# Kernel optimization log

Hardware: AMD Instinct MI355X
Metric: run time of the kernel (lower is better)

Reference implementation:

```python
import jax, jax.numpy as jnp
import numpy as np

N_NODES = 100000
IN_CH = 128
HID = 16
N_EDGES = 3200000


def setup_inputs() -> dict:
    key = jax.random.key(0)
    k1, k2, k3, k4 = jax.random.split(key, 4)
    x = jax.random.normal(k1, (N_NODES, IN_CH), dtype=jnp.float32)
    edge_index = jax.random.randint(k2, (2, N_EDGES), 0, N_NODES, dtype=jnp.int64)
    s1 = 1.0 / np.sqrt(IN_CH)
    s2 = 1.0 / np.sqrt(HID)
    W1 = jax.random.uniform(k3, (IN_CH, HID), dtype=jnp.float32, minval=-s1, maxval=s1)
    b1 = jnp.zeros((HID,), dtype=jnp.float32)
    W2 = jax.random.uniform(k4, (HID, HID), dtype=jnp.float32, minval=-s2, maxval=s2)
    b2 = jnp.zeros((HID,), dtype=jnp.float32)
    return {"x": x, "edge_index": edge_index, "W1": W1, "b1": b1, "W2": W2, "b2": b2}


def _gcn_layer(h, W, b, row, col, norm, n_nodes):
    # GCNConv: transform first (small hidden dim), then normalized sum aggregation
    h = h @ W  # [N, out]
    msg = h[row] * norm[:, None]  # gather over edges incl. self-loops
    out = jax.ops.segment_sum(msg, col, num_segments=n_nodes)
    return out + b


def reference(x, edge_index, W1, b1, W2, b2):
    n = x.shape[0]
    row, col = edge_index[0], edge_index[1]
    # add self-loops (PyG GCNConv default)
    loop = jnp.arange(n, dtype=edge_index.dtype)
    row_l = jnp.concatenate([row, loop])
    col_l = jnp.concatenate([col, loop])
    # symmetric normalization D^-1/2 (A+I) D^-1/2 (degree from target index)
    deg = jax.ops.segment_sum(jnp.ones_like(col_l, dtype=x.dtype), col_l, num_segments=n)
    dinv = jnp.where(deg > 0, jax.lax.rsqrt(deg), 0.0)
    norm = dinv[row_l] * dinv[col_l]

    h = _gcn_layer(x, W1, b1, row_l, col_l, norm, n)
    h = jax.nn.relu(h)  # dropout is identity at eval
    h = _gcn_layer(h, W2, b2, row_l, col_l, norm, n)

    # fused per-edge dot-product link score + sigmoid (original edges only)
    scores = jnp.sum(h[row] * h[col], axis=-1)
    return jax.nn.sigmoid(scores)
```

## Files before the change

kernel.cpp:

```cpp
#include <hip/hip_runtime.h>
#include <hip/hip_bf16.h>
#include <hip/hip_fp16.h>
#include <math.h>


#define BSH 9
#define BSZ 512
#define MAXCH 3200
#define MAXCHUNKS 1024

__global__ __launch_bounds__(512) void pA(const int* __restrict__ col,
                                          int* __restrict__ M, int E, int CH, int NBUK) {
    __shared__ int hist[256];
    const int t = threadIdx.x, b = blockIdx.x;
    if (t < 256) hist[t] = 0;
    __syncthreads();
    const int s = b * CH, e = min(E, s + CH);
    const int n4 = (e - s) >> 2;
    const int4* c4 = (const int4*)(col + s);
    for (int i = t; i < n4; i += 512) {
        int4 c = c4[i];
        atomicAdd(&hist[c.x >> BSH], 1);
        atomicAdd(&hist[c.y >> BSH], 1);
        atomicAdd(&hist[c.z >> BSH], 1);
        atomicAdd(&hist[c.w >> BSH], 1);
    }
    for (int i = s + (n4 << 2) + t; i < e; i += 512) atomicAdd(&hist[col[i] >> BSH], 1);
    __syncthreads();
    for (int i = t; i < NBUK; i += 512) M[b * NBUK + i] = hist[i];
}

__global__ __launch_bounds__(1024) void pB1(int* __restrict__ M, int* __restrict__ T,
                                            int NBUK, int CN) {
    __shared__ int s[1024];
    const int t = threadIdx.x, k = blockIdx.x;
    int own = (t < CN) ? M[t * NBUK + k] : 0;
    s[t] = own;
    __syncthreads();
    for (int d = 1; d < 1024; d <<= 1) {
        int add = (t >= d) ? s[t - d] : 0;
        __syncthreads();
        s[t] += add;
        __syncthreads();
    }
    if (t < CN) M[t * NBUK + k] = s[t] - own;
    if (t == 1023) T[k] = s[1023];
}

__global__ __launch_bounds__(512) void pB2(const int* __restrict__ T, int* __restrict__ S,
                                           int* __restrict__ start, int NBUK, int N, int E) {
    __shared__ int s[512];
    const int t = threadIdx.x;
    int own = (t < NBUK) ? T[t] : 0;
    s[t] = own;
    __syncthreads();
    for (int d = 1; d < 512; d <<= 1) {
        int add = (t >= d) ? s[t - d] : 0;
        __syncthreads();
        s[t] += add;
        __syncthreads();
    }
    if (t < NBUK) S[t] = s[t] - own;
    if (t == 511) S[NBUK] = s[511];
    if (t == 0) start[N] = E;
}

__global__ __launch_bounds__(512) void pC(const int* __restrict__ row, const int* __restrict__ col,
                                          const int* __restrict__ M, const int* __restrict__ S,
                                          unsigned int* __restrict__ ebuf, int E, int CH, int NBUK) {
    __shared__ unsigned int se[MAXCH];
    __shared__ unsigned short pk[MAXCH];
    __shared__ int lhist[256], lbase[256], lcur[256], gbase[256];
    const int t = threadIdx.x, b = blockIdx.x;
    if (t < 256) lhist[t] = 0;
    __syncthreads();
    const int s = b * CH, e = min(E, s + CH);
    const int cnt = e - s;
    const int n4 = cnt >> 2;
    const int4* c4 = (const int4*)(col + s);
    const int4* r4 = (const int4*)(row + s);
    for (int i = t; i < n4; i += 512) {
        int4 c = c4[i];
        atomicAdd(&lhist[c.x >> BSH], 1);
        atomicAdd(&lhist[c.y >> BSH], 1);
        atomicAdd(&lhist[c.z >> BSH], 1);
        atomicAdd(&lhist[c.w >> BSH], 1);
    }
    for (int i = (n4 << 2) + t; i < cnt; i += 512) atomicAdd(&lhist[col[s + i] >> BSH], 1);
    __syncthreads();
    {
        int own = (t < 256) ? lhist[t] : 0;
        if (t < 256) lcur[t] = own;
        __syncthreads();
        for (int d = 1; d < 256; d <<= 1) {
            int add = (t < 256 && t >= d) ? lcur[t - d] : 0;
            __syncthreads();
            if (t < 256) lcur[t] += add;
            __syncthreads();
        }
        if (t < 256) {
            lbase[t] = lcur[t] - own;
            lcur[t] = lcur[t] - own;
        }
        __syncthreads();
        if (t < NBUK) gbase[t] = S[t] + M[b * NBUK + t] - lbase[t];
    }
    __syncthreads();
    for (int i = t; i < n4; i += 512) {
        int4 c = c4[i];
        int4 r = r4[i];
        int k0 = c.x >> BSH, p0 = atomicAdd(&lcur[k0], 1);
        se[p0] = ((unsigned int)(c.x & (BSZ - 1)) << 17) | (unsigned int)r.x; pk[p0] = (unsigned short)k0;
        int k1 = c.y >> BSH, p1 = atomicAdd(&lcur[k1], 1);
        se[p1] = ((unsigned int)(c.y & (BSZ - 1)) << 17) | (unsigned int)r.y; pk[p1] = (unsigned short)k1;
        int k2 = c.z >> BSH, p2 = atomicAdd(&lcur[k2], 1);
        se[p2] = ((unsigned int)(c.z & (BSZ - 1)) << 17) | (unsigned int)r.z; pk[p2] = (unsigned short)k2;
        int k3 = c.w >> BSH, p3 = atomicAdd(&lcur[k3], 1);
        se[p3] = ((unsigned int)(c.w & (BSZ - 1)) << 17) | (unsigned int)r.w; pk[p3] = (unsigned short)k3;
    }
    for (int i = (n4 << 2) + t; i < cnt; i += 512) {
        int c = col[s + i], r = row[s + i];
        int k = c >> BSH, p = atomicAdd(&lcur[k], 1);
        se[p] = ((unsigned int)(c & (BSZ - 1)) << 17) | (unsigned int)r; pk[p] = (unsigned short)k;
    }
    __syncthreads();
    for (int i = t; i < cnt; i += 512) {
        int k = pk[i];
        ebuf[gbase[k] + i] = se[i];
    }
}

__global__ __launch_bounds__(1024) void pC2(const unsigned int* __restrict__ ebuf,
                                            const int* __restrict__ S,
                                            unsigned int* __restrict__ ebuf2,
                                            float* __restrict__ dinv,
                                            int* __restrict__ start, int N) {
    __shared__ int h[BSZ], sc[BSZ], cur[BSZ];
    const int t = threadIdx.x, k = blockIdx.x;
    if (t < BSZ) h[t] = 0;
    __syncthreads();
    const int s = S[k], e = S[k + 1];
    for (int i = s + t; i < e; i += 1024) atomicAdd(&h[ebuf[i] >> 17], 1);
    __syncthreads();
    if (t < BSZ) sc[t] = h[t];
    __syncthreads();
    for (int d = 1; d < BSZ; d <<= 1) {
        int add = (t < BSZ && t >= d) ? sc[t - d] : 0;
        __syncthreads();
        if (t < BSZ) sc[t] += add;
        __syncthreads();
    }
    if (t < BSZ) {
        cur[t] = sc[t] - h[t];
        const int v = (k << BSH) + t;
        if (v < N) {
            dinv[v] = rsqrtf((float)h[t] + 1.0f);
            start[v] = s + cur[t];
        }
    }
    __syncthreads();
    for (int i = s + t; i < e; i += 1024) {
        unsigned int w = ebuf[i];
        int p = atomicAdd(&cur[w >> 17], 1);
        ebuf2[s + p] = w;
    }
}

__global__ __launch_bounds__(256) void k_gemm1(
    const float* __restrict__ x, const float* __restrict__ W1,
    const float* __restrict__ dinv, __half* __restrict__ ts, int N) {
    __shared__ float wsT[16 * 132];
    const int tid = threadIdx.x;
    for (int idx = tid; idx < 2048; idx += 256) {
        int k = idx >> 4, c = idx & 15;
        wsT[c * 132 + k] = W1[idx];
    }
    __syncthreads();
    const int n = blockIdx.x * 256 + tid;
    if (n >= N) return;
    const float4* xr = (const float4*)(x + (size_t)n * 128);
    float acc[16];
    #pragma unroll
    for (int c = 0; c < 16; ++c) acc[c] = 0.f;
    #pragma unroll 4
    for (int k4 = 0; k4 < 32; ++k4) {
        float4 a = xr[k4];
        #pragma unroll
        for (int c = 0; c < 16; ++c) {
            const float4 w = *(const float4*)&wsT[c * 132 + k4 * 4];
            acc[c] = fmaf(a.x, w.x, fmaf(a.y, w.y, fmaf(a.z, w.z, fmaf(a.w, w.w, acc[c]))));
        }
    }
    float dv = dinv[n];
    union { __half h[16]; uint4 u[2]; } o;
    #pragma unroll
    for (int c = 0; c < 16; ++c) o.h[c] = __float2half(acc[c] * dv);
    uint4* dst = (uint4*)(ts + (size_t)n * 16);
    dst[0] = o.u[0]; dst[1] = o.u[1];
}

#define ACC8(q) do {                                         \
    float2 f_;                                               \
    f_ = __half22float2(*(const __half2*)&(q).x); a0 += f_.x; a1 += f_.y; \
    f_ = __half22float2(*(const __half2*)&(q).y); a2 += f_.x; a3 += f_.y; \
    f_ = __half22float2(*(const __half2*)&(q).z); a4 += f_.x; a5 += f_.y; \
    f_ = __half22float2(*(const __half2*)&(q).w); a6 += f_.x; a7 += f_.y; \
} while (0)

__global__ __launch_bounds__(256) void pGat1(
    const unsigned int* __restrict__ ebuf2, const int* __restrict__ start,
    const uint4* __restrict__ tsq, const float* __restrict__ dinv,
    const float* __restrict__ b1, const float* __restrict__ W2,
    uint4* __restrict__ ts2q, int N) {
    __shared__ float w2s[256];
    const int tid = threadIdx.x;
    w2s[tid] = W2[tid];
    __syncthreads();
    const int p = tid & 1;
    const int v = blockIdx.x * 128 + (tid >> 1);
    if (v >= N) return;
    const int s = start[v], e = start[v + 1];
    float a0 = 0.f, a1 = 0.f, a2 = 0.f, a3 = 0.f, a4 = 0.f, a5 = 0.f, a6 = 0.f, a7 = 0.f;
    int i = s;
    for (; i + 8 <= e; i += 8) {
        uint4 q0 = tsq[((size_t)(ebuf2[i    ] & 0x1FFFF) << 1) + p];
        uint4 q1 = tsq[((size_t)(ebuf2[i + 1] & 0x1FFFF) << 1) + p];
        uint4 q2 = tsq[((size_t)(ebuf2[i + 2] & 0x1FFFF) << 1) + p];
        uint4 q3 = tsq[((size_t)(ebuf2[i + 3] & 0x1FFFF) << 1) + p];
        uint4 q4 = tsq[((size_t)(ebuf2[i + 4] & 0x1FFFF) << 1) + p];
        uint4 q5 = tsq[((size_t)(ebuf2[i + 5] & 0x1FFFF) << 1) + p];
        uint4 q6 = tsq[((size_t)(ebuf2[i + 6] & 0x1FFFF) << 1) + p];
        uint4 q7 = tsq[((size_t)(ebuf2[i + 7] & 0x1FFFF) << 1) + p];
        ACC8(q0); ACC8(q1); ACC8(q2); ACC8(q3);
        ACC8(q4); ACC8(q5); ACC8(q6); ACC8(q7);
    }
    for (; i + 4 <= e; i += 4) {
        uint4 q0 = tsq[((size_t)(ebuf2[i    ] & 0x1FFFF) << 1) + p];
        uint4 q1 = tsq[((size_t)(ebuf2[i + 1] & 0x1FFFF) << 1) + p];
        uint4 q2 = tsq[((size_t)(ebuf2[i + 2] & 0x1FFFF) << 1) + p];
        uint4 q3 = tsq[((size_t)(ebuf2[i + 3] & 0x1FFFF) << 1) + p];
        ACC8(q0); ACC8(q1); ACC8(q2); ACC8(q3);
    }
    for (; i < e; ++i) {
        uint4 q0 = tsq[((size_t)(ebuf2[i] & 0x1FFFF) << 1) + p];
        ACC8(q0);
    }
    {
        uint4 sq = tsq[((size_t)v << 1) + p];
        ACC8(sq);
    }
    const float dv = dinv[v];
    const float4 bA = ((const float4*)b1)[2 * p];
    const float4 bB = ((const float4*)b1)[2 * p + 1];
    float h[8];
    h[0] = fmaxf(fmaf(dv, a0, bA.x), 0.f);
    h[1] = fmaxf(fmaf(dv, a1, bA.y), 0.f);
    h[2] = fmaxf(fmaf(dv, a2, bA.z), 0.f);
    h[3] = fmaxf(fmaf(dv, a3, bA.w), 0.f);
    h[4] = fmaxf(fmaf(dv, a4, bB.x), 0.f);
    h[5] = fmaxf(fmaf(dv, a5, bB.y), 0.f);
    h[6] = fmaxf(fmaf(dv, a6, bB.z), 0.f);
    h[7] = fmaxf(fmaf(dv, a7, bB.w), 0.f);
    const int my = p * 8, ot = (1 - p) * 8;
    float o[8];
    #pragma unroll
    for (int c = 0; c < 8; ++c) o[c] = 0.f;
    #pragma unroll
    for (int j = 0; j < 8; ++j) {
        float hm = h[j];
        float ho = __shfl_xor(h[j], 1);
        #pragma unroll
        for (int c = 0; c < 8; ++c) {
            o[c] = fmaf(hm, w2s[(my + j) * 16 + my + c],
                   fmaf(ho, w2s[(ot + j) * 16 + my + c], o[c]));
        }
    }
    union { __half hh[8]; uint4 u; } ov;
    #pragma unroll
    for (int c = 0; c < 8; ++c) ov.hh[c] = __float2half(dv * o[c]);
    ts2q[((size_t)v << 1) + p] = ov.u;
}

__global__ __launch_bounds__(256) void pGat2(
    const unsigned int* __restrict__ ebuf2, const int* __restrict__ start,
    const uint4* __restrict__ tsq, const float* __restrict__ dinv,
    const float* __restrict__ b2, uint4* __restrict__ h2q, int N) {
    const int tid = threadIdx.x;
    const int p = tid & 1;
    const int v = blockIdx.x * 128 + (tid >> 1);
    if (v >= N) return;
    const int s = start[v], e = start[v + 1];
    float a0 = 0.f, a1 = 0.f, a2 = 0.f, a3 = 0.f, a4 = 0.f, a5 = 0.f, a6 = 0.f, a7 = 0.f;
    int i = s;
    for (; i + 8 <= e; i += 8) {
        uint4 q0 = tsq[((size_t)(ebuf2[i    ] & 0x1FFFF) << 1) + p];
        uint4 q1 = tsq[((size_t)(ebuf2[i + 1] & 0x1FFFF) << 1) + p];
        uint4 q2 = tsq[((size_t)(ebuf2[i + 2] & 0x1FFFF) << 1) + p];
        uint4 q3 = tsq[((size_t)(ebuf2[i + 3] & 0x1FFFF) << 1) + p];
        uint4 q4 = tsq[((size_t)(ebuf2[i + 4] & 0x1FFFF) << 1) + p];
        uint4 q5 = tsq[((size_t)(ebuf2[i + 5] & 0x1FFFF) << 1) + p];
        uint4 q6 = tsq[((size_t)(ebuf2[i + 6] & 0x1FFFF) << 1) + p];
        uint4 q7 = tsq[((size_t)(ebuf2[i + 7] & 0x1FFFF) << 1) + p];
        ACC8(q0); ACC8(q1); ACC8(q2); ACC8(q3);
        ACC8(q4); ACC8(q5); ACC8(q6); ACC8(q7);
    }
    for (; i + 4 <= e; i += 4) {
        uint4 q0 = tsq[((size_t)(ebuf2[i    ] & 0x1FFFF) << 1) + p];
        uint4 q1 = tsq[((size_t)(ebuf2[i + 1] & 0x1FFFF) << 1) + p];
        uint4 q2 = tsq[((size_t)(ebuf2[i + 2] & 0x1FFFF) << 1) + p];
        uint4 q3 = tsq[((size_t)(ebuf2[i + 3] & 0x1FFFF) << 1) + p];
        ACC8(q0); ACC8(q1); ACC8(q2); ACC8(q3);
    }
    for (; i < e; ++i) {
        uint4 q0 = tsq[((size_t)(ebuf2[i] & 0x1FFFF) << 1) + p];
        ACC8(q0);
    }
    {
        uint4 sq = tsq[((size_t)v << 1) + p];
        ACC8(sq);
    }
    const float dv = dinv[v];
    const float4 bA = ((const float4*)b2)[2 * p];
    const float4 bB = ((const float4*)b2)[2 * p + 1];
    union { __half hh[8]; uint4 u; } ov;
    ov.hh[0] = __float2half(fmaf(dv, a0, bA.x));
    ov.hh[1] = __float2half(fmaf(dv, a1, bA.y));
    ov.hh[2] = __float2half(fmaf(dv, a2, bA.z));
    ov.hh[3] = __float2half(fmaf(dv, a3, bA.w));
    ov.hh[4] = __float2half(fmaf(dv, a4, bB.x));
    ov.hh[5] = __float2half(fmaf(dv, a5, bB.y));
    ov.hh[6] = __float2half(fmaf(dv, a6, bB.z));
    ov.hh[7] = __float2half(fmaf(dv, a7, bB.w));
    h2q[((size_t)v << 1) + p] = ov.u;
}

__global__ void k_score(const int* __restrict__ row, const int* __restrict__ col,
                        const __half* __restrict__ h2h, float* __restrict__ out, int E) {
    int e = blockIdx.x * 256 + threadIdx.x;
    if (e < E) {
        union { uint4 u[2]; __half2 h[8]; } a, b;
        const uint4* pa = (const uint4*)(h2h + (size_t)row[e] * 16);
        const uint4* pb = (const uint4*)(h2h + (size_t)col[e] * 16);
        a.u[0] = pa[0]; a.u[1] = pa[1];
        b.u[0] = pb[0]; b.u[1] = pb[1];
        float d = 0.f;
        #pragma unroll
        for (int i = 0; i < 8; ++i) {
            float2 fa = __half22float2(a.h[i]);
            float2 fb = __half22float2(b.h[i]);
            d = fmaf(fa.x, fb.x, fmaf(fa.y, fb.y, d));
        }
        out[e] = 1.0f / (1.0f + __expf(-d));
    }
}

__global__ void k_countf(const int* __restrict__ col, float* __restrict__ deg, int E) {
    int e = blockIdx.x * 256 + threadIdx.x;
    if (e < E) atomicAdd(&deg[col[e]], 1.0f);
}
__global__ void k_dinvf(float* __restrict__ dinv, int N) {
    int v = blockIdx.x * 256 + threadIdx.x;
    if (v < N) dinv[v] = rsqrtf(dinv[v] + 1.0f);
}
__global__ __launch_bounds__(256) void k_gemm1f(
    const float* __restrict__ x, const float* __restrict__ W1,
    const float* __restrict__ dinv, float* __restrict__ ts, int N) {
    __shared__ float wsT[16 * 132];
    const int tid = threadIdx.x;
    for (int idx = tid; idx < 2048; idx += 256) {
        int k = idx >> 4, c = idx & 15;
        wsT[c * 132 + k] = W1[idx];
    }
    __syncthreads();
    const int n = blockIdx.x * 256 + tid;
    if (n >= N) return;
    const float4* xr = (const float4*)(x + (size_t)n * 128);
    float acc[16];
    #pragma unroll
    for (int c = 0; c < 16; ++c) acc[c] = 0.f;
    for (int k4 = 0; k4 < 32; ++k4) {
        float4 a = xr[k4];
        #pragma unroll
        for (int c = 0; c < 16; ++c) {
            const float4 w = *(const float4*)&wsT[c * 132 + k4 * 4];
            acc[c] = fmaf(a.x, w.x, fmaf(a.y, w.y, fmaf(a.z, w.z, fmaf(a.w, w.w, acc[c]))));
        }
    }
    float dv = dinv[n];
    float4* o = (float4*)(ts + (size_t)n * 16);
    #pragma unroll
    for (int q = 0; q < 4; ++q)
        o[q] = make_float4(acc[4*q] * dv, acc[4*q+1] * dv, acc[4*q+2] * dv, acc[4*q+3] * dv);
}
__global__ void k_scatter(const int* __restrict__ row, const int* __restrict__ col,
                          const float* __restrict__ ts, float* __restrict__ acc, int E) {
    int g = blockIdx.x * 256 + threadIdx.x;
    int e = g >> 4, c = g & 15;
    if (e < E) atomicAdd(&acc[(size_t)col[e] * 16 + c], ts[(size_t)row[e] * 16 + c]);
}
__global__ void k_finalize(float* __restrict__ acc, const float* __restrict__ ts,
                           const float* __restrict__ dinv, const float* __restrict__ b,
                           int N, int relu) {
    int g = blockIdx.x * 256 + threadIdx.x;
    int v = g >> 4, c = g & 15;
    if (v < N) {
        float h = dinv[v] * (acc[g] + ts[g]) + b[c];
        if (relu) h = fmaxf(h, 0.f);
        acc[g] = h;
    }
}
__global__ __launch_bounds__(256) void k_gemm2f(
    const float* __restrict__ h1, const float* __restrict__ W2,
    const float* __restrict__ dinv, float* __restrict__ ts2, int N) {
    __shared__ float hs[16 * 17];
    __shared__ float ws2[256];
    const int tid = threadIdx.x;
    const int base = blockIdx.x * 16;
    if (tid < 64) ((float4*)ws2)[tid] = ((const float4*)W2)[tid];
    if (tid >= 64 && tid < 128) {
        int t2 = tid - 64;
        float4 v4 = ((const float4*)(h1 + (size_t)base * 16))[t2];
        float* d = &hs[(t2 >> 2) * 17 + (t2 & 3) * 4];
        d[0] = v4.x; d[1] = v4.y; d[2] = v4.z; d[3] = v4.w;
    }
    __syncthreads();
    const int r = tid >> 4, c = tid & 15;
    float a = 0.f;
    #pragma unroll
    for (int kk = 0; kk < 16; ++kk) a = fmaf(hs[r * 17 + kk], ws2[kk * 16 + c], a);
    ts2[(size_t)(base + r) * 16 + c] = a * dinv[base + r];
}
__global__ void k_scoref(const int* __restrict__ row, const int* __restrict__ col,
                         const float* __restrict__ h2, float* __restrict__ out, int E) {
    int e = blockIdx.x * 256 + threadIdx.x;
    if (e < E) {
        const float4* a = (const float4*)(h2 + (size_t)row[e] * 16);
        const float4* b = (const float4*)(h2 + (size_t)col[e] * 16);
        float d = 0.f;
        #pragma unroll
        for (int i = 0; i < 4; ++i) {
            float4 u = a[i], v = b[i];
            d += u.x * v.x + u.y * v.y + u.z * v.z + u.w * v.w;
        }
        out[e] = 1.0f / (1.0f + __expf(-d));
    }
}

extern "C" void kernel_launch(void* const* d_in, const int* in_sizes, int n_in,
                              void* d_out, int out_size, void* d_ws, size_t ws_size,
                              hipStream_t stream) {
    const float* x  = (const float*)d_in[0];
    const int*   ei = (const int*)d_in[1];
    const float* W1 = (const float*)d_in[2];
    const float* b1 = (const float*)d_in[3];
    const float* W2 = (const float*)d_in[4];
    const float* b2 = (const float*)d_in[5];

    const int N = in_sizes[0] / 128;
    const int E = in_sizes[1] / 2;
    const int* row = ei;
    const int* col = ei + E;
    float* out = (float*)d_out;

    const int NBUK = (N + BSZ - 1) / BSZ;
    const int CN = (E + MAXCH - 1) / MAXCH;
    const int CH = MAXCH;

    char* ws = (char*)d_ws;
    size_t off = 0;
    auto alloc = [&](size_t bytes) { void* p = ws + off; off += (bytes + 255) & ~(size_t)255; return p; };
    float*  dinv  = (float*)alloc((size_t)N * 4);
    __half* ts1h  = (__half*)alloc((size_t)N * 32);
    __half* ts2h  = (__half*)alloc((size_t)N * 32);
    int*    start = (int*)alloc((size_t)(N + 1) * 4);
    int*    M     = (int*)alloc((size_t)CN * NBUK * 4);
    int*    T     = (int*)alloc((size_t)NBUK * 4);
    int*    S     = (int*)alloc((size_t)(NBUK + 1) * 4);
    unsigned int* ebuf  = (unsigned int*)alloc((size_t)E * 4);
    unsigned int* ebuf2 = (unsigned int*)alloc((size_t)E * 4);
    const size_t need = off;

    if (N <= 131072 && NBUK <= 256 && CN <= MAXCHUNKS && ws_size >= need) {
        pA <<<CN, 512, 0, stream>>>(col, M, E, CH, NBUK);
        pB1<<<NBUK, 1024, 0, stream>>>(M, T, NBUK, CN);
        pB2<<<1, 512, 0, stream>>>(T, S, start, NBUK, N, E);
        pC <<<CN, 512, 0, stream>>>(row, col, M, S, ebuf, E, CH, NBUK);
        pC2<<<NBUK, 1024, 0, stream>>>(ebuf, S, ebuf2, dinv, start, N);
        k_gemm1<<<(N + 255) / 256, 256, 0, stream>>>(x, W1, dinv, ts1h, N);
        pGat1<<<(N + 127) / 128, 256, 0, stream>>>(ebuf2, start, (const uint4*)ts1h, dinv, b1, W2,
                                                   (uint4*)ts2h, N);
        __half* h2h = ts1h;
        pGat2<<<(N + 127) / 128, 256, 0, stream>>>(ebuf2, start, (const uint4*)ts2h, dinv, b2,
                                                   (uint4*)h2h, N);
        k_score<<<(E + 255) / 256, 256, 0, stream>>>(row, col, h2h, out, E);
    } else {
        float* dinvF = (float*)ws;
        float* ts1F  = (float*)(ws + (size_t)N * 4);
        float* ts2F  = (float*)(ws + (size_t)N * 4 + (size_t)N * 64);
        hipMemsetAsync(dinvF, 0, (size_t)N * 4, stream);
        hipMemsetAsync(ts2F, 0, (size_t)N * 64, stream);
        k_countf<<<(E + 255) / 256, 256, 0, stream>>>(col, dinvF, E);
        k_dinvf<<<(N + 255) / 256, 256, 0, stream>>>(dinvF, N);
        k_gemm1f<<<(N + 255) / 256, 256, 0, stream>>>(x, W1, dinvF, ts1F, N);
        k_scatter<<<(E * 16) / 256, 256, 0, stream>>>(row, col, ts1F, ts2F, E);
        k_finalize<<<(N * 16 + 255) / 256, 256, 0, stream>>>(ts2F, ts1F, dinvF, b1, N, 1);
        k_gemm2f<<<N / 16, 256, 0, stream>>>(ts2F, W2, dinvF, ts1F, N);
        hipMemsetAsync(ts2F, 0, (size_t)N * 64, stream);
        k_scatter<<<(E * 16) / 256, 256, 0, stream>>>(row, col, ts1F, ts2F, E);
        k_finalize<<<(N * 16 + 255) / 256, 256, 0, stream>>>(ts2F, ts1F, dinvF, b2, N, 0);
        k_scoref<<<(E + 255) / 256, 256, 0, stream>>>(row, col, ts2F, out, E);
    }
}
```

Baseline: 262.2 us.

## Replace per-node CSR sort with per-bucket shared-memory atomic aggregation

Drops the second-level per-node sort kernel (pC2) and the second edge buffer. Node degrees now come from global atomics in the bucket-histogram pass, and dinv is computed inside the first GEMM. Both aggregation layers now run one 1024-thread block per 512-node bucket: edge messages are accumulated into a padded shared-memory float array with LDS atomics, then the self-loop, bias, ReLU and W2 transform are applied. This removes a full pass over the edge list and the start-offset array. In exchange it adds 16 shared atomics per edge, random global atomics for degree, only about 196 blocks of parallelism, and a nondeterministic summation order.

After: 991.7 us. +278.3%, slower.

```diff
diff --git a/kernel.cpp b/kernel.cpp
--- a/kernel.cpp
+++ b/kernel.cpp
@@ -6,11 +6,13 @@
 
 #define BSH 9
 #define BSZ 512
+#define ASTR 17
 #define MAXCH 3200
 #define MAXCHUNKS 1024
 
 __global__ __launch_bounds__(512) void pA(const int* __restrict__ col,
-                                          int* __restrict__ M, int E, int CH, int NBUK) {
+                                          int* __restrict__ M, int* __restrict__ degi,
+                                          int E, int CH, int NBUK) {
     __shared__ int hist[256];
     const int t = threadIdx.x, b = blockIdx.x;
     if (t < 256) hist[t] = 0;
@@ -20,12 +22,16 @@
     const int4* c4 = (const int4*)(col + s);
     for (int i = t; i < n4; i += 512) {
         int4 c = c4[i];
-        atomicAdd(&hist[c.x >> BSH], 1);
-        atomicAdd(&hist[c.y >> BSH], 1);
-        atomicAdd(&hist[c.z >> BSH], 1);
-        atomicAdd(&hist[c.w >> BSH], 1);
-    }
-    for (int i = s + (n4 << 2) + t; i < e; i += 512) atomicAdd(&hist[col[i] >> BSH], 1);
+        atomicAdd(&hist[c.x >> BSH], 1); atomicAdd(&degi[c.x], 1);
+        atomicAdd(&hist[c.y >> BSH], 1); atomicAdd(&degi[c.y], 1);
+        atomicAdd(&hist[c.z >> BSH], 1); atomicAdd(&degi[c.z], 1);
+        atomicAdd(&hist[c.w >> BSH], 1); atomicAdd(&degi[c.w], 1);
+    }
+    for (int i = s + (n4 << 2) + t; i < e; i += 512) {
+        int c = col[i];
+        atomicAdd(&hist[c >> BSH], 1);
+        atomicAdd(&degi[c], 1);
+    }
     __syncthreads();
     for (int i = t; i < NBUK; i += 512) M[b * NBUK + i] = hist[i];
 }
@@ -48,7 +54,7 @@
 }
 
 __global__ __launch_bounds__(512) void pB2(const int* __restrict__ T, int* __restrict__ S,
-                                           int* __restrict__ start, int NBUK, int N, int E) {
+                                           int NBUK) {
     __shared__ int s[512];
     const int t = threadIdx.x;
     int own = (t < NBUK) ? T[t] : 0;
@@ -62,7 +68,6 @@
     }
     if (t < NBUK) S[t] = s[t] - own;
     if (t == 511) S[NBUK] = s[511];
-    if (t == 0) start[N] = E;
 }
 
 __global__ __launch_bounds__(512) void pC(const int* __restrict__ row, const int* __restrict__ col,
@@ -130,45 +135,10 @@
     }
 }
 
-__global__ __launch_bounds__(1024) void pC2(const unsigned int* __restrict__ ebuf,
-                                            const int* __restrict__ S,
-                                            unsigned int* __restrict__ ebuf2,
-                                            float* __restrict__ dinv,
-                                            int* __restrict__ start, int N) {
-    __shared__ int h[BSZ], sc[BSZ], cur[BSZ];
-    const int t = threadIdx.x, k = blockIdx.x;
-    if (t < BSZ) h[t] = 0;
-    __syncthreads();
-    const int s = S[k], e = S[k + 1];
-    for (int i = s + t; i < e; i += 1024) atomicAdd(&h[ebuf[i] >> 17], 1);
-    __syncthreads();
-    if (t < BSZ) sc[t] = h[t];
-    __syncthreads();
-    for (int d = 1; d < BSZ; d <<= 1) {
-        int add = (t < BSZ && t >= d) ? sc[t - d] : 0;
-        __syncthreads();
-        if (t < BSZ) sc[t] += add;
-        __syncthreads();
-    }
-    if (t < BSZ) {
-        cur[t] = sc[t] - h[t];
-        const int v = (k << BSH) + t;
-        if (v < N) {
-            dinv[v] = rsqrtf((float)h[t] + 1.0f);
-            start[v] = s + cur[t];
-        }
-    }
-    __syncthreads();
-    for (int i = s + t; i < e; i += 1024) {
-        unsigned int w = ebuf[i];
-        int p = atomicAdd(&cur[w >> 17], 1);
-        ebuf2[s + p] = w;
-    }
-}
-
 __global__ __launch_bounds__(256) void k_gemm1(
     const float* __restrict__ x, const float* __restrict__ W1,
-    const float* __restrict__ dinv, __half* __restrict__ ts, int N) {
+    const int* __restrict__ degi, float* __restrict__ dinv,
+    __half* __restrict__ ts, int N) {
     __shared__ float wsT[16 * 132];
     const int tid = threadIdx.x;
     for (int idx = tid; idx < 2048; idx += 256) {
@@ -191,7 +161,8 @@
             acc[c] = fmaf(a.x, w.x, fmaf(a.y, w.y, fmaf(a.z, w.z, fmaf(a.w, w.w, acc[c]))));
         }
     }
-    float dv = dinv[n];
+    const float dv = rsqrtf((float)degi[n] + 1.0f);
+    dinv[n] = dv;
     union { __half h[16]; uint4 u[2]; } o;
     #pragma unroll
     for (int c = 0; c < 16; ++c) o.h[c] = __float2half(acc[c] * dv);
@@ -199,138 +170,135 @@
     dst[0] = o.u[0]; dst[1] = o.u[1];
 }
 
-#define ACC8(q) do {                                         \
-    float2 f_;                                               \
-    f_ = __half22float2(*(const __half2*)&(q).x); a0 += f_.x; a1 += f_.y; \
-    f_ = __half22float2(*(const __half2*)&(q).y); a2 += f_.x; a3 += f_.y; \
-    f_ = __half22float2(*(const __half2*)&(q).z); a4 += f_.x; a5 += f_.y; \
-    f_ = __half22float2(*(const __half2*)&(q).w); a6 += f_.x; a7 += f_.y; \
+#define ACCAT16(aptr, qa, qb) do {                                                         \
+    float2 f_;                                                                             \
+    f_ = __half22float2(*(const __half2*)&(qa).x); atomicAdd((aptr) + 0,  f_.x); atomicAdd((aptr) + 1,  f_.y); \
+    f_ = __half22float2(*(const __half2*)&(qa).y); atomicAdd((aptr) + 2,  f_.x); atomicAdd((aptr) + 3,  f_.y); \
+    f_ = __half22float2(*(const __half2*)&(qa).z); atomicAdd((aptr) + 4,  f_.x); atomicAdd((aptr) + 5,  f_.y); \
+    f_ = __half22float2(*(const __half2*)&(qa).w); atomicAdd((aptr) + 6,  f_.x); atomicAdd((aptr) + 7,  f_.y); \
+    f_ = __half22float2(*(const __half2*)&(qb).x); atomicAdd((aptr) + 8,  f_.x); atomicAdd((aptr) + 9,  f_.y); \
+    f_ = __half22float2(*(const __half2*)&(qb).y); atomicAdd((aptr) + 10, f_.x); atomicAdd((aptr) + 11, f_.y); \
+    f_ = __half22float2(*(const __half2*)&(qb).z); atomicAdd((aptr) + 12, f_.x); atomicAdd((aptr) + 13, f_.y); \
+    f_ = __half22float2(*(const __half2*)&(qb).w); atomicAdd((aptr) + 14, f_.x); atomicAdd((aptr) + 15, f_.y); \
 } while (0)
 
-__global__ __launch_bounds__(256) void pGat1(
-    const unsigned int* __restrict__ ebuf2, const int* __restrict__ start,
+__global__ __launch_bounds__(1024) void pAgg1(
+    const unsigned int* __restrict__ ebuf, const int* __restrict__ S,
     const uint4* __restrict__ tsq, const float* __restrict__ dinv,
     const float* __restrict__ b1, const float* __restrict__ W2,
     uint4* __restrict__ ts2q, int N) {
+    __shared__ float acc[BSZ * ASTR];
     __shared__ float w2s[256];
-    const int tid = threadIdx.x;
-    w2s[tid] = W2[tid];
-    __syncthreads();
-    const int p = tid & 1;
-    const int v = blockIdx.x * 128 + (tid >> 1);
+    const int t = threadIdx.x, k = blockIdx.x;
+    for (int i = t; i < BSZ * ASTR; i += 1024) acc[i] = 0.f;
+    if (t < 256) w2s[t] = W2[t];
+    __syncthreads();
+    const int s = S[k], e = S[k + 1];
+    int i = s + t;
+    for (; i + 1024 < e; i += 2048) {
+        unsigned int w0 = ebuf[i], w1 = ebuf[i + 1024];
+        const size_t r0 = (size_t)(w0 & 0x1FFFF), r1 = (size_t)(w1 & 0x1FFFF);
+        uint4 qa0 = tsq[r0 << 1], qb0 = tsq[(r0 << 1) + 1];
+        uint4 qa1 = tsq[r1 << 1], qb1 = tsq[(r1 << 1) + 1];
+        float* a0 = &acc[(w0 >> 17) * ASTR];
+        float* a1 = &acc[(w1 >> 17) * ASTR];
+        ACCAT16(a0, qa0, qb0);
+        ACCAT16(a1, qa1, qb1);
+    }
+    if (i < e) {
+        unsigned int w0 = ebuf[i];
+        const size_t r0 = (size_t)(w0 & 0x1FFFF);
+        uint4 qa0 = tsq[r0 << 1], qb0 = tsq[(r0 << 1) + 1];
+        float* a0 = &acc[(w0 >> 17) * ASTR];
+        ACCAT16(a0, qa0, qb0);
+    }
+    __syncthreads();
+    const int lv = t >> 1, p = t & 1;
+    const int v = (k << BSH) + lv;
     if (v >= N) return;
-    const int s = start[v], e = start[v + 1];
-    float a0 = 0.f, a1 = 0.f, a2 = 0.f, a3 = 0.f, a4 = 0.f, a5 = 0.f, a6 = 0.f, a7 = 0.f;
-    int i = s;
-    for (; i + 8 <= e; i += 8) {
-        uint4 q0 = tsq[((size_t)(ebuf2[i    ] & 0x1FFFF) << 1) + p];
-        uint4 q1 = tsq[((size_t)(ebuf2[i + 1] & 0x1FFFF) << 1) + p];
-        uint4 q2 = tsq[((size_t)(ebuf2[i + 2] & 0x1FFFF) << 1) + p];
-        uint4 q3 = tsq[((size_t)(ebuf2[i + 3] & 0x1FFFF) << 1) + p];
-        uint4 q4 = tsq[((size_t)(ebuf2[i + 4] & 0x1FFFF) << 1) + p];
-        uint4 q5 = tsq[((size_t)(ebuf2[i + 5] & 0x1FFFF) << 1) + p];
-        uint4 q6 = tsq[((size_t)(ebuf2[i + 6] & 0x1FFFF) << 1) + p];
-        uint4 q7 = tsq[((size_t)(ebuf2[i + 7] & 0x1FFFF) << 1) + p];
-        ACC8(q0); ACC8(q1); ACC8(q2); ACC8(q3);
-        ACC8(q4); ACC8(q5); ACC8(q6); ACC8(q7);
-    }
-    for (; i + 4 <= e; i += 4) {
-        uint4 q0 = tsq[((size_t)(ebuf2[i    ] & 0x1FFFF) << 1) + p];
-        uint4 q1 = tsq[((size_t)(ebuf2[i + 1] & 0x1FFFF) << 1) + p];
-        uint4 q2 = tsq[((size_t)(ebuf2[i + 2] & 0x1FFFF) << 1) + p];
-        uint4 q3 = tsq[((size_t)(ebuf2[i + 3] & 0x1FFFF) << 1) + p];
-        ACC8(q0); ACC8(q1); ACC8(q2); ACC8(q3);
-    }
-    for (; i < e; ++i) {
-        uint4 q0 = tsq[((size_t)(ebuf2[i] & 0x1FFFF) << 1) + p];
-        ACC8(q0);
-    }
+    const float dv = dinv[v];
+    uint4 sa = tsq[(size_t)v << 1];
+    uint4 sb = tsq[((size_t)v << 1) + 1];
+    const float* ap = &acc[lv * ASTR];
+    float hh[16];
     {
-        uint4 sq = tsq[((size_t)v << 1) + p];
-        ACC8(sq);
-    }
-    const float dv = dinv[v];
-    const float4 bA = ((const float4*)b1)[2 * p];
-    const float4 bB = ((const float4*)b1)[2 * p + 1];
-    float h[8];
-    h[0] = fmaxf(fmaf(dv, a0, bA.x), 0.f);
-    h[1] = fmaxf(fmaf(dv, a1, bA.y), 0.f);
-    h[2] = fmaxf(fmaf(dv, a2, bA.z), 0.f);
-    h[3] = fmaxf(fmaf(dv, a3, bA.w), 0.f);
-    h[4] = fmaxf(fmaf(dv, a4, bB.x), 0.f);
-    h[5] = fmaxf(fmaf(dv, a5, bB.y), 0.f);
-    h[6] = fmaxf(fmaf(dv, a6, bB.z), 0.f);
-    h[7] = fmaxf(fmaf(dv, a7, bB.w), 0.f);
-    const int my = p * 8, ot = (1 - p) * 8;
+        float2 f_;
+        f_ = __half22float2(*(const __half2*)&sa.x); hh[0]  = ap[0]  + f_.x; hh[1]  = ap[1]  + f_.y;
+        f_ = __half22float2(*(const __half2*)&sa.y); hh[2]  = ap[2]  + f_.x; hh[3]  = ap[3]  + f_.y;
+        f_ = __half22float2(*(const __half2*)&sa.z); hh[4]  = ap[4]  + f_.x; hh[5]  = ap[5]  + f_.y;
+        f_ = __half22float2(*(const __half2*)&sa.w); hh[6]  = ap[6]  + f_.x; hh[7]  = ap[7]  + f_.y;
+        f_ = __half22float2(*(const __half2*)&sb.x); hh[8]  = ap[8]  + f_.x; hh[9]  = ap[9]  + f_.y;
+        f_ = __half22float2(*(const __half2*)&sb.y); hh[10] = ap[10] + f_.x; hh[11] = ap[11] + f_.y;
+        f_ = __half22float2(*(const __half2*)&sb.z); hh[12] = ap[12] + f_.x; hh[13] = ap[13] + f_.y;
+        f_ = __half22float2(*(const __half2*)&sb.w); hh[14] = ap[14] + f_.x; hh[15] = ap[15] + f_.y;
+    }
+    #pragma unroll
+    for (int c = 0; c < 16; ++c) hh[c] = fmaxf(fmaf(dv, hh[c], b1[c]), 0.f);
     float o[8];
     #pragma unroll
     for (int c = 0; c < 8; ++c) o[c] = 0.f;
-    #pragma unroll
-    for (int j = 0; j < 8; ++j) {
-        float hm = h[j];
-        float ho = __shfl_xor(h[j], 1);
+    const int cb = 8 * p;
+    #pragma unroll
+    for (int j = 0; j < 16; ++j) {
+        const float hj = hh[j];
         #pragma unroll
-        for (int c = 0; c < 8; ++c) {
-            o[c] = fmaf(hm, w2s[(my + j) * 16 + my + c],
-                   fmaf(ho, w2s[(ot + j) * 16 + my + c], o[c]));
-        }
-    }
-    union { __half hh[8]; uint4 u; } ov;
-    #pragma unroll
-    for (int c = 0; c < 8; ++c) ov.hh[c] = __float2half(dv * o[c]);
+        for (int c = 0; c < 8; ++c) o[c] = fmaf(hj, w2s[j * 16 + cb + c], o[c]);
+    }
+    union { __half h8[8]; uint4 u; } ov;
+    #pragma unroll
+    for (int c = 0; c < 8; ++c) ov.h8[c] = __float2half(dv * o[c]);
     ts2q[((size_t)v << 1) + p] = ov.u;
 }
 
-__global__ __launch_bounds__(256) void pGat2(
-    const unsigned int* __restrict__ ebuf2, const int* __restrict__ start,
+__global__ __launch_bounds__(1024) void pAgg2(
+    const unsigned int* __restrict__ ebuf, const int* __restrict__ S,
     const uint4* __restrict__ tsq, const float* __restrict__ dinv,
     const float* __restrict__ b2, uint4* __restrict__ h2q, int N) {
-    const int tid = threadIdx.x;
-    const int p = tid & 1;
-    const int v = blockIdx.x * 128 + (tid >> 1);
+    __shared__ float acc[BSZ * ASTR];
+    const int t = threadIdx.x, k = blockIdx.x;
+    for (int i = t; i < BSZ * ASTR; i += 1024) acc[i] = 0.f;
+    __syncthreads();
+    const int s = S[k], e = S[k + 1];
+    int i = s + t;
+    for (; i + 1024 < e; i += 2048) {
+        unsigned int w0 = ebuf[i], w1 = ebuf[i + 1024];
+        const size_t r0 = (size_t)(w0 & 0x1FFFF), r1 = (size_t)(w1 & 0x1FFFF);
+        uint4 qa0 = tsq[r0 << 1], qb0 = tsq[(r0 << 1) + 1];
+        uint4 qa1 = tsq[r1 << 1], qb1 = tsq[(r1 << 1) + 1];
+        float* a0 = &acc[(w0 >> 17) * ASTR];
+        float* a1 = &acc[(w1 >> 17) * ASTR];
+        ACCAT16(a0, qa0, qb0);
+        ACCAT16(a1, qa1, qb1);
+    }
+    if (i < e) {
+        unsigned int w0 = ebuf[i];
+        const size_t r0 = (size_t)(w0 & 0x1FFFF);
+        uint4 qa0 = tsq[r0 << 1], qb0 = tsq[(r0 << 1) + 1];
+        float* a0 = &acc[(w0 >> 17) * ASTR];
+        ACCAT16(a0, qa0, qb0);
+    }
+    __syncthreads();
+    const int lv = t >> 1, p = t & 1;
+    const int v = (k << BSH) + lv;
     if (v >= N) return;
-    const int s = start[v], e = start[v + 1];
-    float a0 = 0.f, a1 = 0.f, a2 = 0.f, a3 = 0.f, a4 = 0.f, a5 = 0.f, a6 = 0.f, a7 = 0.f;
-    int i = s;
-    for (; i + 8 <= e; i += 8) {
-        uint4 q0 = tsq[((size_t)(ebuf2[i    ] & 0x1FFFF) << 1) + p];
-        uint4 q1 = tsq[((size_t)(ebuf2[i + 1] & 0x1FFFF) << 1) + p];
-        uint4 q2 = tsq[((size_t)(ebuf2[i + 2] & 0x1FFFF) << 1) + p];
-        uint4 q3 = tsq[((size_t)(ebuf2[i + 3] & 0x1FFFF) << 1) + p];
-        uint4 q4 = tsq[((size_t)(ebuf2[i + 4] & 0x1FFFF) << 1) + p];
-        uint4 q5 = tsq[((size_t)(ebuf2[i + 5] & 0x1FFFF) << 1) + p];
-        uint4 q6 = tsq[((size_t)(ebuf2[i + 6] & 0x1FFFF) << 1) + p];
-        uint4 q7 = tsq[((size_t)(ebuf2[i + 7] & 0x1FFFF) << 1) + p];
-        ACC8(q0); ACC8(q1); ACC8(q2); ACC8(q3);
-        ACC8(q4); ACC8(q5); ACC8(q6); ACC8(q7);
-    }
-    for (; i + 4 <= e; i += 4) {
-        uint4 q0 = tsq[((size_t)(ebuf2[i    ] & 0x1FFFF) << 1) + p];
-        uint4 q1 = tsq[((size_t)(ebuf2[i + 1] & 0x1FFFF) << 1) + p];
-        uint4 q2 = tsq[((size_t)(ebuf2[i + 2] & 0x1FFFF) << 1) + p];
-        uint4 q3 = tsq[((size_t)(ebuf2[i + 3] & 0x1FFFF) << 1) + p];
-        ACC8(q0); ACC8(q1); ACC8(q2); ACC8(q3);
-    }
-    for (; i < e; ++i) {
-        uint4 q0 = tsq[((size_t)(ebuf2[i] & 0x1FFFF) << 1) + p];
-        ACC8(q0);
-    }
-    {
-        uint4 sq = tsq[((size_t)v << 1) + p];
-        ACC8(sq);
-    }
     const float dv = dinv[v];
-    const float4 bA = ((const float4*)b2)[2 * p];
-    const float4 bB = ((const float4*)b2)[2 * p + 1];
-    union { __half hh[8]; uint4 u; } ov;
-    ov.hh[0] = __float2half(fmaf(dv, a0, bA.x));
-    ov.hh[1] = __float2half(fmaf(dv, a1, bA.y));
-    ov.hh[2] = __float2half(fmaf(dv, a2, bA.z));
-    ov.hh[3] = __float2half(fmaf(dv, a3, bA.w));
-    ov.hh[4] = __float2half(fmaf(dv, a4, bB.x));
-    ov.hh[5] = __float2half(fmaf(dv, a5, bB.y));
-    ov.hh[6] = __float2half(fmaf(dv, a6, bB.z));
-    ov.hh[7] = __float2half(fmaf(dv, a7, bB.w));
+    uint4 sq = tsq[((size_t)v << 1) + p];
+    const float* ap = &acc[lv * ASTR + 8 * p];
+    const float* bp = b2 + 8 * p;
+    union { __half h8[8]; uint4 u; } ov;
+    float2 f_;
+    f_ = __half22float2(*(const __half2*)&sq.x);
+    ov.h8[0] = __float2half(fmaf(dv, ap[0] + f_.x, bp[0]));
+    ov.h8[1] = __float2half(fmaf(dv, ap[1] + f_.y, bp[1]));
+    f_ = __half22float2(*(const __half2*)&sq.y);
+    ov.h8[2] = __float2half(fmaf(dv, ap[2] + f_.x, bp[2]));
+    ov.h8[3] = __float2half(fmaf(dv, ap[3] + f_.y, bp[3]));
+    f_ = __half22float2(*(const __half2*)&sq.z);
+    ov.h8[4] = __float2half(fmaf(dv, ap[4] + f_.x, bp[4]));
+    ov.h8[5] = __float2half(fmaf(dv, ap[5] + f_.y, bp[5]));
+    f_ = __half22float2(*(const __half2*)&sq.w);
+    ov.h8[6] = __float2half(fmaf(dv, ap[6] + f_.x, bp[6]));
+    ov.h8[7] = __float2half(fmaf(dv, ap[7] + f_.y, bp[7]));
     h2q[((size_t)v << 1) + p] = ov.u;
 }
 
@@ -472,26 +440,25 @@
     float*  dinv  = (float*)alloc((size_t)N * 4);
     __half* ts1h  = (__half*)alloc((size_t)N * 32);
     __half* ts2h  = (__half*)alloc((size_t)N * 32);
-    int*    start = (int*)alloc((size_t)(N + 1) * 4);
+    int*    degi  = (int*)alloc((size_t)N * 4);
     int*    M     = (int*)alloc((size_t)CN * NBUK * 4);
     int*    T     = (int*)alloc((size_t)NBUK * 4);
     int*    S     = (int*)alloc((size_t)(NBUK + 1) * 4);
     unsigned int* ebuf  = (unsigned int*)alloc((size_t)E * 4);
-    unsigned int* ebuf2 = (unsigned int*)alloc((size_t)E * 4);
     const size_t need = off;
 
     if (N <= 131072 && NBUK <= 256 && CN <= MAXCHUNKS && ws_size >= need) {
-        pA <<<CN, 512, 0, stream>>>(col, M, E, CH, NBUK);
+        hipMemsetAsync(degi, 0, (size_t)N * 4, stream);
+        pA <<<CN, 512, 0, stream>>>(col, M, degi, E, CH, NBUK);
         pB1<<<NBUK, 1024, 0, stream>>>(M, T, NBUK, CN);
-        pB2<<<1, 512, 0, stream>>>(T, S, start, NBUK, N, E);
+        pB2<<<1, 512, 0, stream>>>(T, S, NBUK);
+        k_gemm1<<<(N + 255) / 256, 256, 0, stream>>>(x, W1, degi, dinv, ts1h, N);
         pC <<<CN, 512, 0, stream>>>(row, col, M, S, ebuf, E, CH, NBUK);
-        pC2<<<NBUK, 1024, 0, stream>>>(ebuf, S, ebuf2, dinv, start, N);
-        k_gemm1<<<(N + 255) / 256, 256, 0, stream>>>(x, W1, dinv, ts1h, N);
-        pGat1<<<(N + 127) / 128, 256, 0, stream>>>(ebuf2, start, (const uint4*)ts1h, dinv, b1, W2,
-                                                   (uint4*)ts2h, N);
+        pAgg1<<<NBUK, 1024, 0, stream>>>(ebuf, S, (const uint4*)ts1h, dinv, b1, W2,
+                                         (uint4*)ts2h, N);
         __half* h2h = ts1h;
-        pGat2<<<(N + 127) / 128, 256, 0, stream>>>(ebuf2, start, (const uint4*)ts2h, dinv, b2,
-                                                   (uint4*)h2h, N);
+        pAgg2<<<NBUK, 1024, 0, stream>>>(ebuf, S, (const uint4*)ts2h, dinv, b2,
+                                         (uint4*)h2h, N);
         k_score<<<(E + 255) / 256, 256, 0, stream>>>(row, col, h2h, out, E);
     } else {
         float* dinvF = (float*)ws;
```
